# Performance work log

Measured on AMD Instinct MI355X. Metric: run time of the kernel, lower is better.

Reference implementation:

```python
import jax, jax.numpy as jnp
import numpy as np

N_NODES = 100000
N_EDGES = 1600000
DROP_P = 0.5  # F.dropout default, training=True by default in the source
LRELU_SLOPE = 0.01
EPS = 1e-12


def setup_inputs() -> dict:
    key = jax.random.key(0)
    ks = jax.random.split(key, 8)
    x = jax.random.normal(ks[0], (N_NODES, 64), dtype=jnp.float32)
    edge_index = jax.random.randint(ks[1], (2, N_EDGES), 0, N_NODES, dtype=jnp.int64)
    s = 1.0 / np.sqrt(64)
    W1_l = jax.random.uniform(ks[2], (64, 32), jnp.float32, -s, s)
    W1_r = jax.random.uniform(ks[3], (64, 32), jnp.float32, -s, s)
    b1 = jnp.zeros((32,), jnp.float32)
    s2 = 1.0 / np.sqrt(32)
    W2_l = jax.random.uniform(ks[4], (32, 64), jnp.float32, -s2, s2)
    W2_r = jax.random.uniform(ks[5], (32, 64), jnp.float32, -s2, s2)
    b2 = jnp.zeros((64,), jnp.float32)
    return {"x": x, "edge_index": edge_index, "W1_l": W1_l, "b1": b1,
            "W1_r": W1_r, "W2_l": W2_l, "b2": b2, "W2_r": W2_r}


def _sage_conv(x, src, dst, W_l, b, W_r, n):
    # mean aggregation of source features onto destinations (PyG SAGEConv)
    msg = x[src]                                                 # [E, d]
    agg = jax.ops.segment_sum(msg, dst, num_segments=n)          # [N, d]
    cnt = jax.ops.segment_sum(jnp.ones((src.shape[0],), x.dtype), dst, num_segments=n)
    mean = agg / jnp.maximum(cnt, 1.0)[:, None]
    return mean @ W_l + b + x @ W_r


def _dropout(x, key):
    keep = jax.random.bernoulli(key, 1.0 - DROP_P, x.shape)
    return jnp.where(keep, x / (1.0 - DROP_P), 0.0).astype(x.dtype)


def reference(x, edge_index, W1_l, b1, W1_r, W2_l, b2, W2_r):
    n = x.shape[0]
    src, dst = edge_index[0], edge_index[1]
    dk = jax.random.split(jax.random.key(42), 2)
    h = _sage_conv(x, src, dst, W1_l, b1, W1_r, n)
    h = jax.nn.leaky_relu(h, LRELU_SLOPE)
    h = _dropout(h, dk[0])
    h = _sage_conv(h, src, dst, W2_l, b2, W2_r, n)
    h = _dropout(h, dk[1])
    norm = jnp.sqrt(jnp.sum(h * h, axis=1, keepdims=True))
    return h / jnp.maximum(norm, EPS)
```

## Files before the change

kernel.cpp:

```cpp
#include <hip/hip_runtime.h>

#define N_NODES 100000
#define N_EDGES 1600000
#define NPB 32
#define NB (N_NODES / NPB)
#define CAP 704
#define NCC 49
#define CAPA 34816
#define NFB 64
#define BPC 16

typedef float v2f __attribute__((ext_vector_type(2)));

struct U2 { unsigned a, b; };

__host__ __device__ constexpr U2 tf2x32(unsigned k0, unsigned k1, unsigned c0, unsigned c1) {
  unsigned ks2 = k0 ^ k1 ^ 0x1BD11BDAu;
  unsigned x0 = c0 + k0, x1 = c1 + k1;
#define TFR(r) { x0 += x1; x1 = (x1 << (r)) | (x1 >> (32 - (r))); x1 ^= x0; }
  TFR(13) TFR(15) TFR(26) TFR(6)
  x0 += k1;  x1 += ks2 + 1u;
  TFR(17) TFR(29) TFR(16) TFR(24)
  x0 += ks2; x1 += k0 + 2u;
  TFR(13) TFR(15) TFR(26) TFR(6)
  x0 += k0;  x1 += k1 + 3u;
  TFR(17) TFR(29) TFR(16) TFR(24)
  x0 += k1;  x1 += ks2 + 4u;
  TFR(13) TFR(15) TFR(26) TFR(6)
  x0 += ks2; x1 += k0 + 5u;
#undef TFR
  return U2{x0, x1};
}

constexpr U2 DK0 = tf2x32(0u, 42u, 0u, 0u);
constexpr U2 DK1 = tf2x32(0u, 42u, 0u, 1u);

__device__ __forceinline__ bool keep_bit(unsigned k0, unsigned k1, unsigned j) {
  U2 w = tf2x32(k0, k1, 0u, j);
  return ((w.a ^ w.b) >> 31) == 0u;
}

__device__ __forceinline__ unsigned short f2bf(float f) {
  unsigned u = __float_as_uint(f);
  u += 0x7FFFu + ((u >> 16) & 1u);
  return (unsigned short)(u >> 16);
}
__device__ __forceinline__ v2f up2(unsigned r) {
  v2f v;
  v.x = __uint_as_float(r << 16);
  v.y = __uint_as_float(r & 0xFFFF0000u);
  return v;
}

__global__ __launch_bounds__(256) void k_transform1(
    const float* __restrict__ x, const float* __restrict__ Wl,
    const float* __restrict__ Wr, unsigned short* __restrict__ xlb,
    float* __restrict__ xr) {
  __shared__ __align__(16) float rv[4][64];
  int wid = (int)((blockIdx.x * blockDim.x + threadIdx.x) >> 6);
  int lane = threadIdx.x & 63;
  int wv = (threadIdx.x >> 6) & 3;
  if (wid >= N_NODES) return;
  float xv = x[wid * 64 + lane];
  rv[wv][lane] = xv;
  asm volatile("s_waitcnt lgkmcnt(0)" ::: "memory");
  const float* W = (lane < 32) ? Wl : Wr;
  int c = lane & 31;
  v2f s0 = {0.f, 0.f}, s1 = {0.f, 0.f};
#pragma unroll
  for (int k = 0; k < 64; k += 4) {
    float4 r = *(const float4*)&rv[wv][k];
    v2f w0; w0.x = W[(k + 0) * 32 + c]; w0.y = W[(k + 1) * 32 + c];
    v2f w1; w1.x = W[(k + 2) * 32 + c]; w1.y = W[(k + 3) * 32 + c];
    v2f p0; p0.x = r.x; p0.y = r.y;
    v2f p1; p1.x = r.z; p1.y = r.w;
    s0 += p0 * w0;
    s1 += p1 * w1;
  }
  float s = (s0.x + s0.y) + (s1.x + s1.y);
  if (lane < 32) xlb[wid * 32 + c] = f2bf(s);
  else           xr[wid * 32 + c] = s;
}

__global__ __launch_bounds__(256) void k_binA(
    const int* __restrict__ src, const int* __restrict__ dst,
    int* __restrict__ curA, unsigned* __restrict__ bufA) {
  __shared__ int hist[NCC];
  __shared__ int offsL[NCC + 1];
  __shared__ int baseL[NCC];
  __shared__ int place[NCC];
  __shared__ unsigned stag[2048];
  __shared__ unsigned char cellb[2048];
  int t = threadIdx.x;
  for (long long start = (long long)blockIdx.x * 2048; start < N_EDGES;
       start += (long long)gridDim.x * 2048) {
    int n = (int)min((long long)2048, (long long)N_EDGES - start);
    for (int i = t; i < NCC; i += 256) hist[i] = 0;
    __syncthreads();
    unsigned pv[8]; int pc[8];
#pragma unroll
    for (int i = 0; i < 8; ++i) {
      int idx = t + i * 256;
      if (idx < n) {
        int d = dst[start + idx];
        int s = src[start + idx];
        int cc = d >> 11;
        pc[i] = cc;
        pv[i] = (unsigned)s | ((unsigned)(d & 2047) << 17);
        atomicAdd(&hist[cc], 1);
      } else pc[i] = -1;
    }
    __syncthreads();
    if (t < 64) {
      int lane = t;
      int v = (lane < NCC) ? hist[lane] : 0;
      int x = v;
#pragma unroll
      for (int o = 1; o < 64; o <<= 1) {
        int y = __shfl_up(x, o, 64);
        if (lane >= o) x += y;
      }
      if (lane < NCC) {
        offsL[lane] = x - v;
        place[lane] = 0;
        if (v > 0) baseL[lane] = atomicAdd(&curA[lane], v);
      }
      if (lane == NCC - 1) offsL[NCC] = x;
    }
    __syncthreads();
#pragma unroll
    for (int i = 0; i < 8; ++i) {
      if (pc[i] >= 0) {
        int p = atomicAdd(&place[pc[i]], 1);
        int sl = offsL[pc[i]] + p;
        stag[sl] = pv[i];
        cellb[sl] = (unsigned char)pc[i];
      }
    }
    __syncthreads();
    for (int s2 = t; s2 < n; s2 += 256) {
      int cell = cellb[s2];
      int pos = baseL[cell] + (s2 - offsL[cell]);
      if (pos < CAPA) bufA[(size_t)cell * CAPA + pos] = stag[s2];
    }
    __syncthreads();
  }
}

__global__ __launch_bounds__(256) void k_binB(
    const unsigned* __restrict__ bufA, const int* __restrict__ curA,
    int* __restrict__ cur, unsigned* __restrict__ buf) {
  __shared__ int hist[NFB];
  __shared__ int offsL[NFB + 1];
  __shared__ int baseL[NFB];
  __shared__ int place[NFB];
  __shared__ unsigned stag[2048];
  __shared__ unsigned char cellb[2048];
  int cellc = blockIdx.x / BPC;
  int slice = blockIdx.x % BPC;
  int t = threadIdx.x;
  int cnt = min(curA[cellc], CAPA);
  const unsigned* in = bufA + (size_t)cellc * CAPA;
  for (int start = slice * 2048; start < cnt; start += BPC * 2048) {
    int n = min(2048, cnt - start);
    for (int i = t; i < NFB; i += 256) hist[i] = 0;
    __syncthreads();
    unsigned pv[8]; int pb[8];
#pragma unroll
    for (int i = 0; i < 8; ++i) {
      int idx = t + i * 256;
      if (idx < n) {
        unsigned w = in[start + idx];
        int dlow = (int)(w >> 17);
        int fb = dlow >> 5;
        pb[i] = fb;
        pv[i] = (w & 0x1FFFFu) | ((unsigned)(dlow & 31) << 17);
        atomicAdd(&hist[fb], 1);
      } else pb[i] = -1;
    }
    __syncthreads();
    if (t < 64) {
      int lane = t;
      int v = hist[lane];
      int x = v;
#pragma unroll
      for (int o = 1; o < 64; o <<= 1) {
        int y = __shfl_up(x, o, 64);
        if (lane >= o) x += y;
      }
      offsL[lane] = x - v;
      place[lane] = 0;
      if (v > 0) baseL[lane] = atomicAdd(&cur[cellc * NFB + lane], v);
      if (lane == 63) offsL[NFB] = x;
    }
    __syncthreads();
#pragma unroll
    for (int i = 0; i < 8; ++i) {
      if (pb[i] >= 0) {
        int p = atomicAdd(&place[pb[i]], 1);
        int sl = offsL[pb[i]] + p;
        stag[sl] = pv[i];
        cellb[sl] = (unsigned char)pb[i];
      }
    }
    __syncthreads();
    for (int s2 = t; s2 < n; s2 += 256) {
      int fb = cellb[s2];
      int pos = baseL[fb] + (s2 - offsL[fb]);
      if (pos < CAP) buf[(size_t)(cellc * NFB + fb) * CAP + pos] = stag[s2];
    }
    __syncthreads();
  }
}

__global__ __launch_bounds__(1024) void k_bscan(
    const int* __restrict__ cur, int* __restrict__ bbase) {
  __shared__ int warp_sums[16];
  __shared__ int s_running;
  int t = threadIdx.x;
  int lane = t & 63, w = t >> 6;
  if (t == 0) s_running = 0;
  __syncthreads();
  for (int base = 0; base < NB; base += 1024) {
    int i = base + t;
    int v = (i < NB) ? min(cur[i], CAP) : 0;
    int x = v;
#pragma unroll
    for (int o = 1; o < 64; o <<= 1) {
      int y = __shfl_up(x, o, 64);
      if (lane >= o) x += y;
    }
    if (lane == 63) warp_sums[w] = x;
    __syncthreads();
    if (w == 0) {
      int ws = (lane < 16) ? warp_sums[lane] : 0;
#pragma unroll
      for (int o = 1; o < 16; o <<= 1) {
        int y = __shfl_up(ws, o, 64);
        if (lane >= o) ws += y;
      }
      if (lane < 16) warp_sums[lane] = ws;
    }
    __syncthreads();
    int incl = x + (w > 0 ? warp_sums[w - 1] : 0);
    int excl = s_running + incl - v;
    if (i < NB) bbase[i] = excl;
    __syncthreads();
    if (t == 1023) s_running += incl;
    __syncthreads();
  }
}

__global__ __launch_bounds__(256) void k_bfill(
    const unsigned* __restrict__ buf, const int* __restrict__ cur,
    const int* __restrict__ bbase, int* __restrict__ deg,
    int* __restrict__ offs, int* __restrict__ eidx) {
  __shared__ int ncnt[NPB];
  __shared__ int ncur[NPB];
  __shared__ unsigned sbuf[CAP];
  int b = blockIdx.x, t = threadIdx.x;
  if (t < NPB) ncnt[t] = 0;
  __syncthreads();
  int nb = min(cur[b], CAP);
  const unsigned* bb = buf + (size_t)b * CAP;
  for (int slot = t; slot < nb; slot += 256) {
    unsigned w = bb[slot];
    sbuf[slot] = w;
    atomicAdd(&ncnt[w >> 17], 1);
  }
  __syncthreads();
  if (t < 64) {
    int lane = t;
    int c = (lane < NPB) ? ncnt[lane] : 0;
    int x = c;
#pragma unroll
    for (int o = 1; o < 32; o <<= 1) {
      int y = __shfl_up(x, o, 64);
      if (lane >= o) x += y;
    }
    if (lane < NPB) {
      int excl = x - c;
      ncur[lane] = excl;
      int gn = b * NPB + lane;
      deg[gn] = c;
      offs[gn] = bbase[b] + excl;
    }
  }
  __syncthreads();
  int base = bbase[b];
  for (int slot = t; slot < nb; slot += 256) {
    unsigned w = sbuf[slot];
    int p = atomicAdd(&ncur[w >> 17], 1);
    eidx[base + p] = (int)(w & 0x1FFFF);
  }
}

__global__ __launch_bounds__(256) void k_gather1(
    const unsigned short* __restrict__ xlb, const float* __restrict__ xr,
    const int* __restrict__ offs, const int* __restrict__ deg,
    const int* __restrict__ eidx, const float* __restrict__ b1,
    unsigned short* __restrict__ hpb) {
  int pair = (int)((blockIdx.x * blockDim.x + threadIdx.x) >> 6);
  int lane = threadIdx.x & 63;
  int half = lane >> 5;
  int node = pair * 2 + half;
  if (node >= N_NODES) return;
  int g = (lane >> 3) & 3;
  int ch = lane & 7;
  int c32 = lane & 31;
  int off = offs[node];
  int dg = deg[node];
  float xr_v = xr[node * 32 + c32];
  float b1_v = b1[c32];
  const uint2* x2 = (const uint2*)xlb;
  v2f acc01 = {0.f, 0.f}, acc23 = {0.f, 0.f};
  int k = 0;
  for (; k + 8 <= dg; k += 8) {
    int s0 = eidx[off + k + g];
    int s1 = eidx[off + k + 4 + g];
    uint2 r0 = x2[s0 * 8 + ch];
    uint2 r1 = x2[s1 * 8 + ch];
    acc01 += up2(r0.x); acc23 += up2(r0.y);
    acc01 += up2(r1.x); acc23 += up2(r1.y);
  }
  for (; k < dg; k += 4) {
    if (k + g < dg) {
      int s = eidx[off + k + g];
      uint2 r = x2[s * 8 + ch];
      acc01 += up2(r.x); acc23 += up2(r.y);
    }
  }
  float a0 = acc01.x, a1 = acc01.y, a2 = acc23.x, a3 = acc23.y;
  a0 += __shfl_xor(a0, 8, 64); a0 += __shfl_xor(a0, 16, 64);
  a1 += __shfl_xor(a1, 8, 64); a1 += __shfl_xor(a1, 16, 64);
  a2 += __shfl_xor(a2, 8, 64); a2 += __shfl_xor(a2, 16, 64);
  a3 += __shfl_xor(a3, 8, 64); a3 += __shfl_xor(a3, 16, 64);
  int chunk = c32 >> 2, sub = lane & 3;
  int srcl = (half << 5) + chunk;
  float t0 = __shfl(a0, srcl, 64);
  float t1 = __shfl(a1, srcl, 64);
  float t2 = __shfl(a2, srcl, 64);
  float t3 = __shfl(a3, srcl, 64);
  float val = (sub == 0) ? t0 : (sub == 1) ? t1 : (sub == 2) ? t2 : t3;
  float inv = 1.0f / fmaxf((float)dg, 1.0f);
  int j = node * 32 + c32;
  float v = val * inv + b1_v + xr_v;
  v = (v > 0.f) ? v : 0.01f * v;
  float h = keep_bit(DK0.a, DK0.b, (unsigned)j) ? 2.0f * v : 0.0f;
  hpb[j] = f2bf(h);
}

__global__ __launch_bounds__(256) void k_out(
    const unsigned short* __restrict__ hpb, const int* __restrict__ offs,
    const int* __restrict__ deg, const int* __restrict__ eidx,
    const float* __restrict__ W2l, const float* __restrict__ b2,
    const float* __restrict__ W2r, float* __restrict__ out) {
  __shared__ __align__(16) float rv[4][64];
  int wid = (int)((blockIdx.x * blockDim.x + threadIdx.x) >> 6);
  int lane = threadIdx.x & 63;
  int wv = (threadIdx.x >> 6) & 3;
  if (wid >= N_NODES) return;
  int g = lane >> 3, ch = lane & 7;
  int off = offs[wid];
  int dg = deg[wid];
  const uint2* h2 = (const uint2*)hpb;
  uint2 own = h2[wid * 8 + ch];
  float bias = b2[lane];
  v2f acc01 = {0.f, 0.f}, acc23 = {0.f, 0.f};
  int k = 0;
  for (; k + 16 <= dg; k += 16) {
    int s0 = eidx[off + k + g];
    int s1 = eidx[off + k + 8 + g];
    uint2 r0 = h2[s0 * 8 + ch];
    uint2 r1 = h2[s1 * 8 + ch];
    acc01 += up2(r0.x); acc23 += up2(r0.y);
    acc01 += up2(r1.x); acc23 += up2(r1.y);
  }
  for (; k < dg; k += 8) {
    if (k + g < dg) {
      int s = eidx[off + k + g];
      uint2 r = h2[s * 8 + ch];
      acc01 += up2(r.x); acc23 += up2(r.y);
    }
  }
  float a0 = acc01.x, a1 = acc01.y, a2 = acc23.x, a3 = acc23.y;
  a0 += __shfl_xor(a0, 8, 64); a0 += __shfl_xor(a0, 16, 64); a0 += __shfl_xor(a0, 32, 64);
  a1 += __shfl_xor(a1, 8, 64); a1 += __shfl_xor(a1, 16, 64); a1 += __shfl_xor(a1, 32, 64);
  a2 += __shfl_xor(a2, 8, 64); a2 += __shfl_xor(a2, 16, 64); a2 += __shfl_xor(a2, 32, 64);
  a3 += __shfl_xor(a3, 8, 64); a3 += __shfl_xor(a3, 16, 64); a3 += __shfl_xor(a3, 32, 64);
  float inv = 1.0f / fmaxf((float)dg, 1.0f);
  if (lane < 8) {
    float4 v;
    v.x = a0 * inv; v.y = a1 * inv; v.z = a2 * inv; v.w = a3 * inv;
    *(float4*)&rv[wv][lane * 4] = v;
  } else if (lane < 16) {
    float4 v;
    v.x = __uint_as_float(own.x << 16);
    v.y = __uint_as_float(own.x & 0xFFFF0000u);
    v.z = __uint_as_float(own.y << 16);
    v.w = __uint_as_float(own.y & 0xFFFF0000u);
    *(float4*)&rv[wv][32 + (lane - 8) * 4] = v;
  }
  asm volatile("s_waitcnt lgkmcnt(0)" ::: "memory");
  v2f sa = {0.f, 0.f}, sb = {0.f, 0.f};
#pragma unroll
  for (int kk = 0; kk < 32; kk += 4) {
    float4 r1 = *(const float4*)&rv[wv][kk];
    float4 r2 = *(const float4*)&rv[wv][32 + kk];
    v2f w0; w0.x = W2l[(kk + 0) * 64 + lane]; w0.y = W2l[(kk + 1) * 64 + lane];
    v2f w1; w1.x = W2l[(kk + 2) * 64 + lane]; w1.y = W2l[(kk + 3) * 64 + lane];
    v2f u0; u0.x = W2r[(kk + 0) * 64 + lane]; u0.y = W2r[(kk + 1) * 64 + lane];
    v2f u1; u1.x = W2r[(kk + 2) * 64 + lane]; u1.y = W2r[(kk + 3) * 64 + lane];
    v2f p0; p0.x = r1.x; p0.y = r1.y;
    v2f p1; p1.x = r1.z; p1.y = r1.w;
    v2f q0; q0.x = r2.x; q0.y = r2.y;
    v2f q1; q1.x = r2.z; q1.y = r2.w;
    sa += p0 * w0;  sa += p1 * w1;
    sb += q0 * u0;  sb += q1 * u1;
  }
  float v = (sa.x + sa.y) + (sb.x + sb.y) + bias;
  unsigned j = (unsigned)(wid * 64 + lane);
  float d = keep_bit(DK1.a, DK1.b, j) ? 2.0f * v : 0.0f;
  float ss = d * d;
#pragma unroll
  for (int o = 32; o > 0; o >>= 1) ss += __shfl_xor(ss, o, 64);
  float scale = 1.0f / fmaxf(sqrtf(ss), 1e-12f);
  out[j] = d * scale;
}

extern "C" void kernel_launch(void* const* d_in, const int* in_sizes, int n_in,
                              void* d_out, int out_size, void* d_ws, size_t ws_size,
                              hipStream_t stream) {
  const float* x   = (const float*)d_in[0];
  const int*   ei  = (const int*)d_in[1];
  const float* W1l = (const float*)d_in[2];
  const float* b1  = (const float*)d_in[3];
  const float* W1r = (const float*)d_in[4];
  const float* W2l = (const float*)d_in[5];
  const float* b2  = (const float*)d_in[6];
  const float* W2r = (const float*)d_in[7];
  float* out = (float*)d_out;

  const int* src = ei;
  const int* dst = ei + N_EDGES;

  const size_t F32 = (size_t)N_NODES * 32;
  char* w = (char*)d_ws;
  unsigned* bufA = (unsigned*)w;
  float* xr      = (float*)w;
  w += F32 * sizeof(float);
  unsigned* buf  = (unsigned*)w;
  unsigned short* xlb = (unsigned short*)w;
  unsigned short* hpb = xlb + F32;
  w += F32 * 2 * sizeof(unsigned short);
  int* curA  = (int*)w; w += NCC * sizeof(int);
  int* cur   = (int*)w; w += NB * sizeof(int);
  int* bbase = (int*)w; w += NB * sizeof(int);
  int* deg   = (int*)w; w += N_NODES * sizeof(int);
  int* offs  = (int*)w; w += N_NODES * sizeof(int);
  int* eidx  = (int*)w;

  hipMemsetAsync(curA, 0, (size_t)(NCC + NB) * sizeof(int), stream);

  k_binA<<<(N_EDGES + 2047) / 2048, 256, 0, stream>>>(src, dst, curA, bufA);
  k_binB<<<NCC * BPC, 256, 0, stream>>>(bufA, curA, cur, buf);
  k_bscan<<<1, 1024, 0, stream>>>(cur, bbase);
  k_bfill<<<NB, 256, 0, stream>>>(buf, cur, bbase, deg, offs, eidx);

  k_transform1<<<(N_NODES + 3) / 4, 256, 0, stream>>>(x, W1l, W1r, xlb, xr);
  k_gather1<<<(N_NODES / 2 + 3) / 4, 256, 0, stream>>>(xlb, xr, offs, deg, eidx, b1, hpb);
  k_out<<<(N_NODES + 3) / 4, 256, 0, stream>>>(hpb, offs, deg, eidx, W2l, b2, W2r, out);
}
```

Measured before the change: 286.4 us.

## Precompute dropout masks in a separate kernel and register-cache transform weights

```diff
diff --git a/kernel.cpp b/kernel.cpp
--- a/kernel.cpp
+++ b/kernel.cpp
@@ -9,6 +9,8 @@
 #define CAPA 34816
 #define NFB 64
 #define BPC 16
+#define M1W 50000
+#define M2W 100000
 
 typedef float v2f __attribute__((ext_vector_type(2)));
 
@@ -52,34 +54,53 @@
   return v;
 }
 
-__global__ __launch_bounds__(256) void k_transform1(
+__global__ __launch_bounds__(256) void k_mask(unsigned long long* __restrict__ msk) {
+  int w = (int)((blockIdx.x * blockDim.x + threadIdx.x) >> 6);
+  int lane = threadIdx.x & 63;
+  int nw = (int)((gridDim.x * blockDim.x) >> 6);
+  for (; w < M1W + M2W; w += nw) {
+    unsigned k0, k1, j;
+    if (w < M1W) { k0 = DK0.a; k1 = DK0.b; j = (unsigned)w * 64u + (unsigned)lane; }
+    else { k0 = DK1.a; k1 = DK1.b; j = (unsigned)(w - M1W) * 64u + (unsigned)lane; }
+    unsigned long long bits = __ballot(keep_bit(k0, k1, j));
+    if (lane == 0) msk[w] = bits;
+  }
+}
+
+__global__ __launch_bounds__(256, 4) void k_transform1(
     const float* __restrict__ x, const float* __restrict__ Wl,
     const float* __restrict__ Wr, unsigned short* __restrict__ xlb,
     float* __restrict__ xr) {
   __shared__ __align__(16) float rv[4][64];
-  int wid = (int)((blockIdx.x * blockDim.x + threadIdx.x) >> 6);
   int lane = threadIdx.x & 63;
   int wv = (threadIdx.x >> 6) & 3;
-  if (wid >= N_NODES) return;
-  float xv = x[wid * 64 + lane];
-  rv[wv][lane] = xv;
-  asm volatile("s_waitcnt lgkmcnt(0)" ::: "memory");
   const float* W = (lane < 32) ? Wl : Wr;
   int c = lane & 31;
-  v2f s0 = {0.f, 0.f}, s1 = {0.f, 0.f};
-#pragma unroll
-  for (int k = 0; k < 64; k += 4) {
-    float4 r = *(const float4*)&rv[wv][k];
-    v2f w0; w0.x = W[(k + 0) * 32 + c]; w0.y = W[(k + 1) * 32 + c];
-    v2f w1; w1.x = W[(k + 2) * 32 + c]; w1.y = W[(k + 3) * 32 + c];
-    v2f p0; p0.x = r.x; p0.y = r.y;
-    v2f p1; p1.x = r.z; p1.y = r.w;
-    s0 += p0 * w0;
-    s1 += p1 * w1;
-  }
-  float s = (s0.x + s0.y) + (s1.x + s1.y);
-  if (lane < 32) xlb[wid * 32 + c] = f2bf(s);
-  else           xr[wid * 32 + c] = s;
+  float w[64];
+#pragma unroll
+  for (int k = 0; k < 64; ++k) w[k] = W[k * 32 + c];
+  int wid0 = (int)((blockIdx.x * blockDim.x + threadIdx.x) >> 6);
+  int wstride = (int)((gridDim.x * blockDim.x) >> 6);
+  for (int wid = wid0; wid < N_NODES; wid += wstride) {
+    float xv = x[wid * 64 + lane];
+    asm volatile("s_waitcnt lgkmcnt(0)" ::: "memory");
+    rv[wv][lane] = xv;
+    asm volatile("s_waitcnt lgkmcnt(0)" ::: "memory");
+    v2f s0 = {0.f, 0.f}, s1 = {0.f, 0.f};
+#pragma unroll
+    for (int k = 0; k < 64; k += 4) {
+      float4 r = *(const float4*)&rv[wv][k];
+      v2f w0; w0.x = w[k + 0]; w0.y = w[k + 1];
+      v2f w1; w1.x = w[k + 2]; w1.y = w[k + 3];
+      v2f p0; p0.x = r.x; p0.y = r.y;
+      v2f p1; p1.x = r.z; p1.y = r.w;
+      s0 += p0 * w0;
+      s1 += p1 * w1;
+    }
+    float s = (s0.x + s0.y) + (s1.x + s1.y);
+    if (lane < 32) xlb[wid * 32 + c] = f2bf(s);
+    else           xr[wid * 32 + c] = s;
+  }
 }
 
 __global__ __launch_bounds__(256) void k_binA(
@@ -299,6 +320,7 @@
     const unsigned short* __restrict__ xlb, const float* __restrict__ xr,
     const int* __restrict__ offs, const int* __restrict__ deg,
     const int* __restrict__ eidx, const float* __restrict__ b1,
+    const unsigned long long* __restrict__ msk1,
     unsigned short* __restrict__ hpb) {
   int pair = (int)((blockIdx.x * blockDim.x + threadIdx.x) >> 6);
   int lane = threadIdx.x & 63;
@@ -312,6 +334,7 @@
   int dg = deg[node];
   float xr_v = xr[node * 32 + c32];
   float b1_v = b1[c32];
+  unsigned long long mw = msk1[pair];
   const uint2* x2 = (const uint2*)xlb;
   v2f acc01 = {0.f, 0.f}, acc23 = {0.f, 0.f};
   int k = 0;
@@ -346,7 +369,7 @@
   int j = node * 32 + c32;
   float v = val * inv + b1_v + xr_v;
   v = (v > 0.f) ? v : 0.01f * v;
-  float h = keep_bit(DK0.a, DK0.b, (unsigned)j) ? 2.0f * v : 0.0f;
+  float h = ((mw >> lane) & 1ull) ? 2.0f * v : 0.0f;
   hpb[j] = f2bf(h);
 }
 
@@ -354,7 +377,8 @@
     const unsigned short* __restrict__ hpb, const int* __restrict__ offs,
     const int* __restrict__ deg, const int* __restrict__ eidx,
     const float* __restrict__ W2l, const float* __restrict__ b2,
-    const float* __restrict__ W2r, float* __restrict__ out) {
+    const float* __restrict__ W2r, const unsigned long long* __restrict__ msk2,
+    float* __restrict__ out) {
   __shared__ __align__(16) float rv[4][64];
   int wid = (int)((blockIdx.x * blockDim.x + threadIdx.x) >> 6);
   int lane = threadIdx.x & 63;
@@ -366,6 +390,7 @@
   const uint2* h2 = (const uint2*)hpb;
   uint2 own = h2[wid * 8 + ch];
   float bias = b2[lane];
+  unsigned long long mw = msk2[wid];
   v2f acc01 = {0.f, 0.f}, acc23 = {0.f, 0.f};
   int k = 0;
   for (; k + 16 <= dg; k += 16) {
@@ -419,13 +444,12 @@
     sb += q0 * u0;  sb += q1 * u1;
   }
   float v = (sa.x + sa.y) + (sb.x + sb.y) + bias;
-  unsigned j = (unsigned)(wid * 64 + lane);
-  float d = keep_bit(DK1.a, DK1.b, j) ? 2.0f * v : 0.0f;
+  float d = ((mw >> lane) & 1ull) ? 2.0f * v : 0.0f;
   float ss = d * d;
 #pragma unroll
   for (int o = 32; o > 0; o >>= 1) ss += __shfl_xor(ss, o, 64);
   float scale = 1.0f / fmaxf(sqrtf(ss), 1e-12f);
-  out[j] = d * scale;
+  out[(size_t)wid * 64 + lane] = d * scale;
 }
 
 extern "C" void kernel_launch(void* const* d_in, const int* in_sizes, int n_in,
@@ -458,16 +482,18 @@
   int* bbase = (int*)w; w += NB * sizeof(int);
   int* deg   = (int*)w; w += N_NODES * sizeof(int);
   int* offs  = (int*)w; w += N_NODES * sizeof(int);
-  int* eidx  = (int*)w;
+  int* eidx  = (int*)w; w += (size_t)N_EDGES * sizeof(int);
+  unsigned long long* msk = (unsigned long long*)w;
 
   hipMemsetAsync(curA, 0, (size_t)(NCC + NB) * sizeof(int), stream);
 
+  k_mask<<<2048, 256, 0, stream>>>(msk);
   k_binA<<<(N_EDGES + 2047) / 2048, 256, 0, stream>>>(src, dst, curA, bufA);
   k_binB<<<NCC * BPC, 256, 0, stream>>>(bufA, curA, cur, buf);
   k_bscan<<<1, 1024, 0, stream>>>(cur, bbase);
   k_bfill<<<NB, 256, 0, stream>>>(buf, cur, bbase, deg, offs, eidx);
 
-  k_transform1<<<(N_NODES + 3) / 4, 256, 0, stream>>>(x, W1l, W1r, xlb, xr);
-  k_gather1<<<(N_NODES / 2 + 3) / 4, 256, 0, stream>>>(xlb, xr, offs, deg, eidx, b1, hpb);
-  k_out<<<(N_NODES + 3) / 4, 256, 0, stream>>>(hpb, offs, deg, eidx, W2l, b2, W2r, out);
-}
+  k_transform1<<<1024, 256, 0, stream>>>(x, W1l, W1r, xlb, xr);
+  k_gather1<<<(N_NODES / 2 + 3) / 4, 256, 0, stream>>>(xlb, xr, offs, deg, eidx, b1, msk, hpb);
+  k_out<<<(N_NODES + 3) / 4, 256, 0, stream>>>(hpb, offs, deg, eidx, W2l, b2, W2r, msk + M1W, out);
+}
```

Result: no change. 281.4 us (-1.7%).

## Register-cache weights in persistent transform; prefetch edge indices via lane shuffles

Applied to the files above, without the earlier changes.

```diff
diff --git a/kernel.cpp b/kernel.cpp
--- a/kernel.cpp
+++ b/kernel.cpp
@@ -52,34 +52,40 @@
   return v;
 }
 
-__global__ __launch_bounds__(256) void k_transform1(
+__global__ __launch_bounds__(256, 4) void k_transform1(
     const float* __restrict__ x, const float* __restrict__ Wl,
     const float* __restrict__ Wr, unsigned short* __restrict__ xlb,
     float* __restrict__ xr) {
   __shared__ __align__(16) float rv[4][64];
-  int wid = (int)((blockIdx.x * blockDim.x + threadIdx.x) >> 6);
   int lane = threadIdx.x & 63;
   int wv = (threadIdx.x >> 6) & 3;
-  if (wid >= N_NODES) return;
-  float xv = x[wid * 64 + lane];
-  rv[wv][lane] = xv;
-  asm volatile("s_waitcnt lgkmcnt(0)" ::: "memory");
   const float* W = (lane < 32) ? Wl : Wr;
   int c = lane & 31;
-  v2f s0 = {0.f, 0.f}, s1 = {0.f, 0.f};
-#pragma unroll
-  for (int k = 0; k < 64; k += 4) {
-    float4 r = *(const float4*)&rv[wv][k];
-    v2f w0; w0.x = W[(k + 0) * 32 + c]; w0.y = W[(k + 1) * 32 + c];
-    v2f w1; w1.x = W[(k + 2) * 32 + c]; w1.y = W[(k + 3) * 32 + c];
-    v2f p0; p0.x = r.x; p0.y = r.y;
-    v2f p1; p1.x = r.z; p1.y = r.w;
-    s0 += p0 * w0;
-    s1 += p1 * w1;
-  }
-  float s = (s0.x + s0.y) + (s1.x + s1.y);
-  if (lane < 32) xlb[wid * 32 + c] = f2bf(s);
-  else           xr[wid * 32 + c] = s;
+  float w[64];
+#pragma unroll
+  for (int k = 0; k < 64; ++k) w[k] = W[k * 32 + c];
+  int wid0 = (int)((blockIdx.x * blockDim.x + threadIdx.x) >> 6);
+  int wstride = (int)((gridDim.x * blockDim.x) >> 6);
+  for (int wid = wid0; wid < N_NODES; wid += wstride) {
+    float xv = x[wid * 64 + lane];
+    asm volatile("s_waitcnt lgkmcnt(0)" ::: "memory");
+    rv[wv][lane] = xv;
+    asm volatile("s_waitcnt lgkmcnt(0)" ::: "memory");
+    v2f s0 = {0.f, 0.f}, s1 = {0.f, 0.f};
+#pragma unroll
+    for (int k = 0; k < 64; k += 4) {
+      float4 r = *(const float4*)&rv[wv][k];
+      v2f w0; w0.x = w[k + 0]; w0.y = w[k + 1];
+      v2f w1; w1.x = w[k + 2]; w1.y = w[k + 3];
+      v2f p0; p0.x = r.x; p0.y = r.y;
+      v2f p1; p1.x = r.z; p1.y = r.w;
+      s0 += p0 * w0;
+      s1 += p1 * w1;
+    }
+    float s = (s0.x + s0.y) + (s1.x + s1.y);
+    if (lane < 32) xlb[wid * 32 + c] = f2bf(s);
+    else           xr[wid * 32 + c] = s;
+  }
 }
 
 __global__ __launch_bounds__(256) void k_binA(
@@ -312,16 +318,26 @@
   int dg = deg[node];
   float xr_v = xr[node * 32 + c32];
   float b1_v = b1[c32];
+  int sidx = eidx[(dg > 0) ? (off + min(c32, dg - 1)) : 0];
+  int hb = half << 5;
   const uint2* x2 = (const uint2*)xlb;
   v2f acc01 = {0.f, 0.f}, acc23 = {0.f, 0.f};
+  int kmax = min(dg, 32);
   int k = 0;
-  for (; k + 8 <= dg; k += 8) {
-    int s0 = eidx[off + k + g];
-    int s1 = eidx[off + k + 4 + g];
-    uint2 r0 = x2[s0 * 8 + ch];
-    uint2 r1 = x2[s1 * 8 + ch];
+  for (; k + 8 <= kmax; k += 8) {
+    int i0 = __shfl(sidx, hb + k + g, 64);
+    int i1 = __shfl(sidx, hb + k + 4 + g, 64);
+    uint2 r0 = x2[i0 * 8 + ch];
+    uint2 r1 = x2[i1 * 8 + ch];
     acc01 += up2(r0.x); acc23 += up2(r0.y);
     acc01 += up2(r1.x); acc23 += up2(r1.y);
+  }
+  for (; k < kmax; k += 4) {
+    int i = __shfl(sidx, hb + min(k + g, kmax - 1), 64);
+    if (k + g < kmax) {
+      uint2 r = x2[i * 8 + ch];
+      acc01 += up2(r.x); acc23 += up2(r.y);
+    }
   }
   for (; k < dg; k += 4) {
     if (k + g < dg) {
@@ -336,7 +352,7 @@
   a2 += __shfl_xor(a2, 8, 64); a2 += __shfl_xor(a2, 16, 64);
   a3 += __shfl_xor(a3, 8, 64); a3 += __shfl_xor(a3, 16, 64);
   int chunk = c32 >> 2, sub = lane & 3;
-  int srcl = (half << 5) + chunk;
+  int srcl = hb + chunk;
   float t0 = __shfl(a0, srcl, 64);
   float t1 = __shfl(a1, srcl, 64);
   float t2 = __shfl(a2, srcl, 64);
@@ -366,15 +382,24 @@
   const uint2* h2 = (const uint2*)hpb;
   uint2 own = h2[wid * 8 + ch];
   float bias = b2[lane];
+  int sidx = eidx[(dg > 0) ? (off + min(lane, dg - 1)) : 0];
   v2f acc01 = {0.f, 0.f}, acc23 = {0.f, 0.f};
+  int kmax = min(dg, 64);
   int k = 0;
-  for (; k + 16 <= dg; k += 16) {
-    int s0 = eidx[off + k + g];
-    int s1 = eidx[off + k + 8 + g];
-    uint2 r0 = h2[s0 * 8 + ch];
-    uint2 r1 = h2[s1 * 8 + ch];
+  for (; k + 16 <= kmax; k += 16) {
+    int i0 = __shfl(sidx, k + g, 64);
+    int i1 = __shfl(sidx, k + 8 + g, 64);
+    uint2 r0 = h2[i0 * 8 + ch];
+    uint2 r1 = h2[i1 * 8 + ch];
     acc01 += up2(r0.x); acc23 += up2(r0.y);
     acc01 += up2(r1.x); acc23 += up2(r1.y);
+  }
+  for (; k < kmax; k += 8) {
+    int i = __shfl(sidx, min(k + g, kmax - 1), 64);
+    if (k + g < kmax) {
+      uint2 r = h2[i * 8 + ch];
+      acc01 += up2(r.x); acc23 += up2(r.y);
+    }
   }
   for (; k < dg; k += 8) {
     if (k + g < dg) {
@@ -467,7 +492,7 @@
   k_bscan<<<1, 1024, 0, stream>>>(cur, bbase);
   k_bfill<<<NB, 256, 0, stream>>>(buf, cur, bbase, deg, offs, eidx);
 
-  k_transform1<<<(N_NODES + 3) / 4, 256, 0, stream>>>(x, W1l, W1r, xlb, xr);
+  k_transform1<<<1024, 256, 0, stream>>>(x, W1l, W1r, xlb, xr);
   k_gather1<<<(N_NODES / 2 + 3) / 4, 256, 0, stream>>>(xlb, xr, offs, deg, eidx, b1, hpb);
   k_out<<<(N_NODES + 3) / 4, 256, 0, stream>>>(hpb, offs, deg, eidx, W2l, b2, W2r, out);
 }
```

New measurement: 253.9 us (median of 2 runs). 1.13x faster.
